# Kernel optimization log

Hardware: AMD Instinct MI355X
Metric: run time of the kernel (lower is better)

The kernel has to match this reference:

```python
import jax, jax.numpy as jnp
import numpy as np

B, S, HID = 2, 2048, 1024
H, HKV, D = 16, 8, 128
G = H // HKV  # GQA group size
EPS = 1e-6
THETA = 1000000.0


def setup_inputs() -> dict:
    key = jax.random.key(0)
    ks = jax.random.split(key, 6)
    hidden_states = jax.random.normal(ks[0], (B, S, HID), dtype=jnp.float32)
    # causal boolean mask: True = attend
    attention_mask = jnp.tril(jnp.ones((S, S), dtype=bool))[None, None]
    # RoPE tables (HF convention: freqs duplicated across both halves)
    inv_freq = 1.0 / (THETA ** (jnp.arange(0, D, 2, dtype=jnp.float32) / D))
    ang = jnp.arange(S, dtype=jnp.float32)[:, None] * inv_freq[None, :]  # [S, D/2]
    emb = jnp.concatenate([ang, ang], axis=-1)  # [S, D]
    cos, sin = jnp.cos(emb), jnp.sin(emb)
    std = 0.02
    Wq = jax.random.normal(ks[1], (HID, H * D), dtype=jnp.float32) * std
    Wk = jax.random.normal(ks[2], (HID, HKV * D), dtype=jnp.float32) * std
    Wv = jax.random.normal(ks[3], (HID, HKV * D), dtype=jnp.float32) * std
    Wo = jax.random.normal(ks[4], (H * D, HID), dtype=jnp.float32) * std
    q_norm_w = jnp.ones((D,), dtype=jnp.float32)
    k_norm_w = jnp.ones((D,), dtype=jnp.float32)
    return {"hidden_states": hidden_states, "attention_mask": attention_mask,
            "cos": cos, "sin": sin, "Wq": Wq, "Wk": Wk, "Wv": Wv, "Wo": Wo,
            "q_norm_w": q_norm_w, "k_norm_w": k_norm_w}


def _rms_norm(x, w):
    var = jnp.mean(x * x, axis=-1, keepdims=True)
    return x * jax.lax.rsqrt(var + EPS) * w


def _rotate_half(x):
    x1, x2 = jnp.split(x, 2, axis=-1)
    return jnp.concatenate([-x2, x1], axis=-1)


def reference(hidden_states, attention_mask, cos, sin, Wq, Wk, Wv, Wo, q_norm_w, k_norm_w):
    b, s, _ = hidden_states.shape
    xq = (hidden_states @ Wq).reshape(b, s, H, D).transpose(0, 2, 1, 3)    # [B,H,S,D]
    xk = (hidden_states @ Wk).reshape(b, s, HKV, D).transpose(0, 2, 1, 3)  # [B,Hkv,S,D]
    xv = (hidden_states @ Wv).reshape(b, s, HKV, D).transpose(0, 2, 1, 3)  # [B,Hkv,S,D]
    xq = _rms_norm(xq, q_norm_w)
    xk = _rms_norm(xk, k_norm_w)
    c = cos[None, None]  # [1,1,S,D]
    si = sin[None, None]
    xq = xq * c + _rotate_half(xq) * si
    xk = xk * c + _rotate_half(xk) * si
    # GQA without materializing repeated KV: group q heads per kv head
    xqg = xq.reshape(b, HKV, G, s, D)
    scale = 1.0 / jnp.sqrt(jnp.asarray(D, dtype=xq.dtype))
    scores = jnp.einsum('bkgsd,bktd->bkgst', xqg, xk) * scale  # [B,Hkv,G,S,S]
    mask = attention_mask[:, :, None]  # [1,1,1,S,S]
    scores = jnp.where(mask, scores, jnp.asarray(-jnp.inf, dtype=scores.dtype))
    probs = jax.nn.softmax(scores, axis=-1)
    out = jnp.einsum('bkgst,bktd->bkgsd', probs, xv)  # [B,Hkv,G,S,D]
    out = out.reshape(b, H, s, D).transpose(0, 2, 1, 3).reshape(b, s, H * D)
    return out @ Wo
```

## Files before the change

### kernel.cpp

```cpp
#include <hip/hip_runtime.h>
#include <stdint.h>

#define B_ 2
#define S_ 2048
#define H_ 16
#define HKV_ 8
#define D_ 128
#define EPS_ 1e-6f
#define SCALE_ 0.08838834764831845f
#define KVSTRIDE_ 262144

typedef __attribute__((ext_vector_type(8))) __bf16 bf16x8;
typedef __attribute__((ext_vector_type(4))) float f32x4;
typedef __attribute__((ext_vector_type(16))) float f32x16;

static __device__ __forceinline__ uint16_t f2b(float f) {
  uint32_t u = __builtin_bit_cast(uint32_t, f);
  u += 0x7fffu + ((u >> 16) & 1u);
  return (uint16_t)(u >> 16);
}
static __device__ __forceinline__ float b2f(uint16_t b) {
  uint32_t u = ((uint32_t)b) << 16;
  return __builtin_bit_cast(float, u);
}

typedef const __attribute__((address_space(1))) uint32_t* gas_p;
typedef __attribute__((address_space(3))) uint32_t* las_p;
static __device__ __forceinline__ void gload16(const void* g, void* l) {
  __builtin_amdgcn_global_load_lds((gas_p)g, (las_p)l, 16, 0, 0);
}

__global__ __launch_bounds__(256) void prep(const float* __restrict__ hidden,
                                            uint16_t* __restrict__ Xb,
                                            const float* __restrict__ Wq,
                                            const float* __restrict__ Wk,
                                            const float* __restrict__ Wv,
                                            const float* __restrict__ Wo,
                                            uint16_t* __restrict__ Wqt,
                                            uint16_t* __restrict__ Wkt,
                                            uint16_t* __restrict__ Wvt,
                                            uint16_t* __restrict__ Wot) {
  __shared__ float tt[32][33];
  int bid = blockIdx.x;
  if (bid < 4096) {
    int i = bid * 256 + threadIdx.x;
    float4 f = ((const float4*)hidden)[i];
    uint2 o;
    o.x = (uint32_t)f2b(f.x) | ((uint32_t)f2b(f.y) << 16);
    o.y = (uint32_t)f2b(f.z) | ((uint32_t)f2b(f.w) << 16);
    ((uint2*)Xb)[i] = o;
    return;
  }
  bid -= 4096;
  const float* src; uint16_t* dst; int K, N, bx, by;
  if (bid < 2048)       { src = Wq; dst = Wqt; K = 1024; N = 2048; bx = bid & 63; by = bid >> 6; }
  else if (bid < 3072)  { bid -= 2048; src = Wk; dst = Wkt; K = 1024; N = 1024; bx = bid & 31; by = bid >> 5; }
  else if (bid < 4096)  { bid -= 3072; src = Wv; dst = Wvt; K = 1024; N = 1024; bx = bid & 31; by = bid >> 5; }
  else                  { bid -= 4096; src = Wo; dst = Wot; K = 2048; N = 1024; bx = bid & 31; by = bid >> 5; }
  int nb = bx * 32, kb = by * 32;
  int tx = threadIdx.x & 31, ty = threadIdx.x >> 5;
  #pragma unroll
  for (int i = ty; i < 32; i += 8) tt[i][tx] = src[(size_t)(kb + i) * N + nb + tx];
  __syncthreads();
  #pragma unroll
  for (int i = ty; i < 32; i += 8) dst[(size_t)(nb + i) * K + kb + tx] = f2b(tt[tx][i]);
}

__global__ __launch_bounds__(256) void gemm_qkv(const uint16_t* __restrict__ A,
                                                const uint16_t* __restrict__ Bt,
                                                uint16_t* __restrict__ Qb,
                                                uint16_t* __restrict__ Kb,
                                                uint16_t* __restrict__ Vtb,
                                                const float* __restrict__ qw,
                                                const float* __restrict__ kw,
                                                const float* __restrict__ cosr,
                                                const float* __restrict__ sinr) {
  __shared__ uint16_t Sh[128 * 128];
  uint16_t* Al = Sh;
  uint16_t* Bl = Sh + 128 * 64;
  int tid = threadIdx.x;
  int lane = tid & 63, lr = lane & 15, g = lane >> 4;
  int w = tid >> 6, wm = w >> 1, wn = w & 1;
  int wbase = w * 64;
  int m0 = blockIdx.y * 128, n0 = blockIdx.x * 128;
  f32x4 acc[4][4] = {};
  for (int k0 = 0; k0 < 1024; k0 += 64) {
    __syncthreads();
    #pragma unroll
    for (int p = 0; p < 4; ++p) {
      int c = tid + p * 256;
      int row = c >> 3, cb = c & 7;
      int sc = (cb ^ (row & 7)) * 8;
      gload16(A + (size_t)(m0 + row) * 1024 + k0 + sc, Al + (size_t)(p * 256 + wbase) * 8);
      gload16(Bt + (size_t)(n0 + row) * 1024 + k0 + sc, Bl + (size_t)(p * 256 + wbase) * 8);
    }
    __syncthreads();
    #pragma unroll
    for (int ks = 0; ks < 2; ++ks) {
      bf16x8 af[4], bfr[4];
      #pragma unroll
      for (int mi = 0; mi < 4; ++mi) {
        int row = wm * 64 + mi * 16 + lr;
        af[mi] = *(bf16x8*)((char*)Al + row * 128 + ((ks * 64 + g * 16) ^ ((row & 7) << 4)));
      }
      #pragma unroll
      for (int ni = 0; ni < 4; ++ni) {
        int row = wn * 64 + ni * 16 + lr;
        bfr[ni] = *(bf16x8*)((char*)Bl + row * 128 + ((ks * 64 + g * 16) ^ ((row & 7) << 4)));
      }
      __builtin_amdgcn_s_setprio(1);
      #pragma unroll
      for (int mi = 0; mi < 4; ++mi)
        #pragma unroll
        for (int ni = 0; ni < 4; ++ni)
          acc[mi][ni] = __builtin_amdgcn_mfma_f32_16x16x32_bf16(af[mi], bfr[ni], acc[mi][ni], 0, 0, 0);
      __builtin_amdgcn_s_setprio(0);
    }
  }
  __syncthreads();
  uint16_t* L = Sh;
  #pragma unroll
  for (int mi = 0; mi < 4; ++mi)
    #pragma unroll
    for (int ni = 0; ni < 4; ++ni)
      #pragma unroll
      for (int e = 0; e < 4; ++e) {
        int row = wm * 64 + mi * 16 + 4 * g + e;
        int col = wn * 64 + ni * 16 + lr;
        L[row * 128 + ((((col >> 3) ^ (row & 7)) << 3) | (col & 7))] = f2b(acc[mi][ni][e]);
      }
  __syncthreads();
  int hsel = n0 >> 7;
  if (hsel < 24) {
    int row = tid >> 1, half = tid & 1;
    int gr = m0 + row, bb = gr >> 11, s = gr & 2047;
    int d0 = half * 32;
    float x[64];
    #pragma unroll
    for (int c8 = 0; c8 < 8; ++c8) {
      int jj = (c8 & 3) * 8 + d0 + (c8 >> 2) * 64;
      union { bf16x8 v; uint16_t u[8]; } tmp;
      tmp.v = *(bf16x8*)(L + row * 128 + (((jj >> 3) ^ (row & 7)) << 3));
      #pragma unroll
      for (int k = 0; k < 8; ++k) x[c8 * 8 + k] = b2f(tmp.u[k]);
    }
    float ss = 0.f;
    #pragma unroll
    for (int k = 0; k < 64; ++k) ss += x[k] * x[k];
    ss += __shfl_xor(ss, 1, 64);
    float rn = rsqrtf(ss * (1.0f / 128.0f) + EPS_);
    const float* wv = (hsel < 16) ? qw : kw;
    float scq = (hsel < 16) ? SCALE_ : 1.0f;
    rn *= scq;
    uint16_t* outp = (hsel < 16)
      ? Qb + (((size_t)(bb * 16 + hsel)) * 2048 + s) * 128
      : Kb + (((size_t)(bb * 8 + (hsel - 16))) * 2048 + s) * 128;
    const float* cR = cosr + s * 128;
    const float* sR = sinr + s * 128;
    #pragma unroll
    for (int c = 0; c < 4; ++c) {
      int dlo = d0 + c * 8;
      uint16_t olo[8], ohi[8];
      #pragma unroll
      for (int k = 0; k < 8; ++k) {
        int d = dlo + k;
        float x1 = x[c * 8 + k] * rn * wv[d];
        float x2 = x[32 + c * 8 + k] * rn * wv[d + 64];
        olo[k] = f2b(x1 * cR[d] - x2 * sR[d]);
        ohi[k] = f2b(x2 * cR[d + 64] + x1 * sR[d + 64]);
      }
      *(uint4*)(outp + dlo) = *(uint4*)olo;
      *(uint4*)(outp + 64 + dlo) = *(uint4*)ohi;
    }
  } else {
    int kvh = hsel - 24;
    int d0 = tid >> 1, sh = tid & 1;
    int bb = m0 >> 11, sg0 = (m0 & 2047) + sh * 64;
    union { uint16_t u[64]; uint4 q[8]; } vv;
    #pragma unroll
    for (int sl = 0; sl < 64; ++sl) {
      int srow = sh * 64 + sl;
      vv.u[sl] = L[srow * 128 + ((((d0 >> 3) ^ (srow & 7)) << 3) | (d0 & 7))];
    }
    uint16_t* vt = Vtb + (((size_t)(bb * 8 + kvh)) * 128 + d0) * 2048 + sg0;
    #pragma unroll
    for (int c = 0; c < 8; ++c) *(uint4*)(vt + c * 8) = vv.q[c];
  }
}

__global__ __launch_bounds__(256) void vrepack(const uint16_t* __restrict__ Vt,
                                               uint16_t* __restrict__ Vp) {
  int bkv = blockIdx.y, p = blockIdx.x;
  const uint16_t* src = Vt + (size_t)bkv * KVSTRIDE_;
  uint16_t* dst = Vp + (size_t)bkv * KVSTRIDE_;
  #pragma unroll
  for (int i = 0; i < 16; ++i) {
    int idx = i * 256 + threadIdx.x;
    int d = idx >> 5, sc = p * 32 + (idx & 31);
    int s8 = sc * 8;
    uint4 v = *(const uint4*)(src + (size_t)d * 2048 + s8);
    int kb64 = s8 >> 6, j = (s8 >> 4) & 3, hh = (s8 >> 3) & 1;
    int dt = d >> 5, qlv = d & 31;
    ((uint4*)dst)[(kb64 * 16 + dt * 4 + j) * 64 + hh * 32 + qlv] = v;
  }
}

__global__ __launch_bounds__(256) void gemm_o(const uint16_t* __restrict__ A,
                                              const uint16_t* __restrict__ Bt,
                                              float* __restrict__ Cout,
                                              int M, int N, int K) {
  __shared__ uint16_t Al[128 * 64];
  __shared__ uint16_t Bl[64 * 64];
  int tid = threadIdx.x;
  int lane = tid & 63, lr = lane & 15, g = lane >> 4;
  int w = tid >> 6, wm = w >> 1, wn = w & 1;
  int wbase = w * 64;
  int m0 = blockIdx.y * 128, n0 = blockIdx.x * 64;
  f32x4 acc[4][2] = {};
  for (int k0 = 0; k0 < K; k0 += 64) {
    __syncthreads();
    #pragma unroll
    for (int p = 0; p < 4; ++p) {
      int c = tid + p * 256;
      int row = c >> 3, cb = c & 7;
      int sc = (cb ^ (row & 7)) * 8;
      gload16(A + (size_t)(m0 + row) * K + k0 + sc, Al + (size_t)(p * 256 + wbase) * 8);
    }
    #pragma unroll
    for (int p = 0; p < 2; ++p) {
      int c = tid + p * 256;
      int row = c >> 3, cb = c & 7;
      int sc = (cb ^ (row & 7)) * 8;
      gload16(Bt + (size_t)(n0 + row) * K + k0 + sc, Bl + (size_t)(p * 256 + wbase) * 8);
    }
    __syncthreads();
    #pragma unroll
    for (int ks = 0; ks < 2; ++ks) {
      bf16x8 af[4], bfr[2];
      #pragma unroll
      for (int mi = 0; mi < 4; ++mi) {
        int row = wm * 64 + mi * 16 + lr;
        af[mi] = *(bf16x8*)((char*)Al + row * 128 + ((ks * 64 + g * 16) ^ ((row & 7) << 4)));
      }
      #pragma unroll
      for (int ni = 0; ni < 2; ++ni) {
        int row = wn * 32 + ni * 16 + lr;
        bfr[ni] = *(bf16x8*)((char*)Bl + row * 128 + ((ks * 64 + g * 16) ^ ((row & 7) << 4)));
      }
      __builtin_amdgcn_s_setprio(1);
      #pragma unroll
      for (int mi = 0; mi < 4; ++mi)
        #pragma unroll
        for (int ni = 0; ni < 2; ++ni)
          acc[mi][ni] = __builtin_amdgcn_mfma_f32_16x16x32_bf16(af[mi], bfr[ni], acc[mi][ni], 0, 0, 0);
      __builtin_amdgcn_s_setprio(0);
    }
  }
  #pragma unroll
  for (int mi = 0; mi < 4; ++mi)
    #pragma unroll
    for (int ni = 0; ni < 2; ++ni)
      #pragma unroll
      for (int e = 0; e < 4; ++e) {
        int row = m0 + wm * 64 + mi * 16 + 4 * g + e;
        int col = n0 + wn * 32 + ni * 16 + lr;
        Cout[(size_t)row * N + col] = acc[mi][ni][e];
      }
}

#define STAGE(BUF, KB) {                                                       \
  int kb64 = (KB) * 64;                                                        \
  _Pragma("unroll") for (int p2 = 0; p2 < 4; ++p2) {                           \
    int ck = p2 * 4 + w;                                                       \
    int krow = ck * 4 + (lane >> 4);                                           \
    int kg = (lane & 15) ^ (krow & 7);                                         \
    gload16(Kg + (size_t)(kb64 + krow) * D_ + kg * 8, Kl[BUF] + ck * 512);     \
  } }

__global__ __launch_bounds__(256, 2) void attn_kernel(const uint16_t* __restrict__ Qb,
                                                      const uint16_t* __restrict__ Kb,
                                                      const uint16_t* __restrict__ Vp,
                                                      uint16_t* __restrict__ out) {
  __shared__ uint16_t Kl[2][64 * 128];
  int tid = threadIdx.x, lane = tid & 63, w = tid >> 6;
  int ql = lane & 31, hi = lane >> 5;
  int bi = blockIdx.x;
  int biH = bi >> 8;
  int j2 = bi & 255;
  int qgl = j2 >> 5;
  int qg = biH ? qgl : 15 - qgl;
  int rem = j2 & 31;
  int bkv = rem >> 1, hsel = rem & 1;
  int b = bkv >> 3, kv = bkv & 7, h = kv * 2 + hsel;
  int qt = qg * 4 + w;
  int q0 = qt * 32;
  int mykb = qt >> 1;
  int kbmax = 2 * qg + 1;
  const uint16_t* Qg = Qb + ((size_t)(b * H_ + h)) * S_ * D_;
  const uint16_t* Kg = Kb + ((size_t)(b * HKV_ + kv)) * S_ * D_;
  const uint16_t* Vpg = Vp + (size_t)(b * HKV_ + kv) * KVSTRIDE_;
  bf16x8 qf[8];
  #pragma unroll
  for (int t = 0; t < 8; ++t)
    qf[t] = *(const bf16x8*)(Qg + (size_t)(q0 + ql) * D_ + t * 16 + 8 * hi);
  f32x16 O[4] = {};
  float mrun = -__builtin_inff();
  float lrun = 0.f;
  STAGE(0, 0)
  for (int kb = 0; kb <= kbmax; ++kb) {
    int cur = kb & 1;
    __syncthreads();
    if (kb < kbmax) STAGE(cur ^ 1, kb + 1)
    if (kb <= mykb) {
      const uint16_t* KlC = Kl[cur];
      const uint16_t* Vb64 = Vpg + (size_t)kb * 8192;
      bool diag = (kb == mykb);
      bool skip2 = diag && ((qt & 1) == 0);
      float p0[16], p1[16];
      {
        bf16x8 kf[8];
        #pragma unroll
        for (int t = 0; t < 8; ++t)
          kf[t] = *(const bf16x8*)(KlC + ql * 128 + (((2 * t + hi) ^ (ql & 7)) * 8));
        f32x16 acc = {};
        __builtin_amdgcn_s_setprio(1);
        #pragma unroll
        for (int t = 0; t < 8; ++t)
          acc = __builtin_amdgcn_mfma_f32_32x32x16_bf16(kf[t], qf[t], acc, 0, 0, 0);
        __builtin_amdgcn_s_setprio(0);
        #pragma unroll
        for (int r = 0; r < 16; ++r) p0[r] = acc[r];
      }
      if (!skip2) {
        bf16x8 kf[8];
        #pragma unroll
        for (int t = 0; t < 8; ++t)
          kf[t] = *(const bf16x8*)(KlC + (32 + ql) * 128 + (((2 * t + hi) ^ (ql & 7)) * 8));
        f32x16 acc = {};
        __builtin_amdgcn_s_setprio(1);
        #pragma unroll
        for (int t = 0; t < 8; ++t)
          acc = __builtin_amdgcn_mfma_f32_32x32x16_bf16(kf[t], qf[t], acc, 0, 0, 0);
        __builtin_amdgcn_s_setprio(0);
        #pragma unroll
        for (int r = 0; r < 16; ++r) p1[r] = acc[r];
      }
      bf16x8 vf[16];
      #pragma unroll
      for (int dt = 0; dt < 4; ++dt) {
        vf[dt * 4 + 0] = *(const bf16x8*)(Vb64 + ((dt * 4 + 0) * 64 + lane) * 8);
        vf[dt * 4 + 1] = *(const bf16x8*)(Vb64 + ((dt * 4 + 1) * 64 + lane) * 8);
      }
      if (!skip2) {
        #pragma unroll
        for (int dt = 0; dt < 4; ++dt) {
          vf[dt * 4 + 2] = *(const bf16x8*)(Vb64 + ((dt * 4 + 2) * 64 + lane) * 8);
          vf[dt * 4 + 3] = *(const bf16x8*)(Vb64 + ((dt * 4 + 3) * 64 + lane) * 8);
        }
      }
      if (diag && !(qt & 1)) {
        #pragma unroll
        for (int r = 0; r < 16; ++r) {
          int kk = kb * 64 + 8 * (r >> 2) + 4 * hi + (r & 3);
          if (kk > q0 + ql) p0[r] = -__builtin_inff();
        }
      }
      if (diag && (qt & 1)) {
        #pragma unroll
        for (int r = 0; r < 16; ++r) {
          int kk = kb * 64 + 32 + 8 * (r >> 2) + 4 * hi + (r & 3);
          if (kk > q0 + ql) p1[r] = -__builtin_inff();
        }
      }
      float m8[8];
      #pragma unroll
      for (int i = 0; i < 8; ++i) m8[i] = fmaxf(p0[i], p0[i + 8]);
      if (!skip2) {
        #pragma unroll
        for (int i = 0; i < 8; ++i) m8[i] = fmaxf(m8[i], fmaxf(p1[i], p1[i + 8]));
      }
      float m4a = fmaxf(m8[0], m8[4]), m4b = fmaxf(m8[1], m8[5]);
      float m4c = fmaxf(m8[2], m8[6]), m4d = fmaxf(m8[3], m8[7]);
      float pmax = fmaxf(fmaxf(m4a, m4b), fmaxf(m4c, m4d));
      pmax = fmaxf(pmax, __shfl_xor(pmax, 32, 64));
      if (__any(pmax > mrun + 8.f)) {
        float mnew = fmaxf(mrun, pmax);
        float rs = __expf(mrun - mnew);
        lrun *= rs;
        #pragma unroll
        for (int r = 0; r < 16; ++r) {
          float rr = __shfl(rs, (r & 3) + 8 * (r >> 2) + 4 * hi, 64);
          #pragma unroll
          for (int dt = 0; dt < 4; ++dt) O[dt][r] *= rr;
        }
        mrun = mnew;
      }
      float ls = 0.f;
      union PW { uint32_t w[4]; bf16x8 v; } pa0, pa1;
      #pragma unroll
      for (int r = 0; r < 16; ++r) { p0[r] = __expf(p0[r] - mrun); ls += p0[r]; }
      {
        uint32_t uu[4][2];
        #pragma unroll
        for (int T = 0; T < 4; ++T) {
          asm("v_cvt_pk_bf16_f32 %0, %1, %2" : "=v"(uu[T][0]) : "v"(p0[4 * T]), "v"(p0[4 * T + 1]));
          asm("v_cvt_pk_bf16_f32 %0, %1, %2" : "=v"(uu[T][1]) : "v"(p0[4 * T + 2]), "v"(p0[4 * T + 3]));
        }
        uint32_t a = uu[0][0], bb2 = uu[1][0];
        asm("v_permlane32_swap_b32 %0, %1" : "+v"(a), "+v"(bb2));
        uint32_t c = uu[0][1], d = uu[1][1];
        asm("v_permlane32_swap_b32 %0, %1" : "+v"(c), "+v"(d));
        pa0.w[0] = a; pa0.w[1] = c; pa0.w[2] = bb2; pa0.w[3] = d;
        uint32_t a2 = uu[2][0], b2 = uu[3][0];
        asm("v_permlane32_swap_b32 %0, %1" : "+v"(a2), "+v"(b2));
        uint32_t c2 = uu[2][1], d2 = uu[3][1];
        asm("v_permlane32_swap_b32 %0, %1" : "+v"(c2), "+v"(d2));
        pa1.w[0] = a2; pa1.w[1] = c2; pa1.w[2] = b2; pa1.w[3] = d2;
      }
      __builtin_amdgcn_s_setprio(1);
      #pragma unroll
      for (int dt = 0; dt < 4; ++dt) {
        O[dt] = __builtin_amdgcn_mfma_f32_32x32x16_bf16(pa0.v, vf[dt * 4 + 0], O[dt], 0, 0, 0);
        O[dt] = __builtin_amdgcn_mfma_f32_32x32x16_bf16(pa1.v, vf[dt * 4 + 1], O[dt], 0, 0, 0);
      }
      __builtin_amdgcn_s_setprio(0);
      if (!skip2) {
        union PW pa2, pa3;
        #pragma unroll
        for (int r = 0; r < 16; ++r) { p1[r] = __expf(p1[r] - mrun); ls += p1[r]; }
        {
          uint32_t uu[4][2];
          #pragma unroll
          for (int T = 0; T < 4; ++T) {
            asm("v_cvt_pk_bf16_f32 %0, %1, %2" : "=v"(uu[T][0]) : "v"(p1[4 * T]), "v"(p1[4 * T + 1]));
            asm("v_cvt_pk_bf16_f32 %0, %1, %2" : "=v"(uu[T][1]) : "v"(p1[4 * T + 2]), "v"(p1[4 * T + 3]));
          }
          uint32_t a = uu[0][0], bb2 = uu[1][0];
          asm("v_permlane32_swap_b32 %0, %1" : "+v"(a), "+v"(bb2));
          uint32_t c = uu[0][1], d = uu[1][1];
          asm("v_permlane32_swap_b32 %0, %1" : "+v"(c), "+v"(d));
          pa2.w[0] = a; pa2.w[1] = c; pa2.w[2] = bb2; pa2.w[3] = d;
          uint32_t a2 = uu[2][0], b2 = uu[3][0];
          asm("v_permlane32_swap_b32 %0, %1" : "+v"(a2), "+v"(b2));
          uint32_t c2 = uu[2][1], d2 = uu[3][1];
          asm("v_permlane32_swap_b32 %0, %1" : "+v"(c2), "+v"(d2));
          pa3.w[0] = a2; pa3.w[1] = c2; pa3.w[2] = b2; pa3.w[3] = d2;
        }
        __builtin_amdgcn_s_setprio(1);
        #pragma unroll
        for (int dt = 0; dt < 4; ++dt) {
          O[dt] = __builtin_amdgcn_mfma_f32_32x32x16_bf16(pa2.v, vf[dt * 4 + 2], O[dt], 0, 0, 0);
          O[dt] = __builtin_amdgcn_mfma_f32_32x32x16_bf16(pa3.v, vf[dt * 4 + 3], O[dt], 0, 0, 0);
        }
        __builtin_amdgcn_s_setprio(0);
      }
      ls += __shfl_xor(ls, 32, 64);
      lrun += ls;
    }
  }
  float linv = 1.0f / lrun;
  #pragma unroll
  for (int r = 0; r < 16; ++r) {
    int qrl = (r & 3) + 8 * (r >> 2) + 4 * hi;
    float lr_ = __shfl(linv, qrl, 64);
    #pragma unroll
    for (int dt = 0; dt < 4; ++dt) {
      size_t o = ((size_t)(b * S_ + q0 + qrl)) * 2048 + h * 128 + dt * 32 + ql;
      out[o] = f2b(O[dt][r] * lr_);
    }
  }
}

extern "C" void kernel_launch(void* const* d_in, const int* in_sizes, int n_in,
                              void* d_out, int out_size, void* d_ws, size_t ws_size,
                              hipStream_t stream) {
  const float* hidden = (const float*)d_in[0];
  const float* cosr = (const float*)d_in[2];
  const float* sinr = (const float*)d_in[3];
  const float* Wq = (const float*)d_in[4];
  const float* Wk = (const float*)d_in[5];
  const float* Wv = (const float*)d_in[6];
  const float* Wo = (const float*)d_in[7];
  const float* qw = (const float*)d_in[8];
  const float* kw = (const float*)d_in[9];

  uint16_t* p = (uint16_t*)d_ws;
  uint16_t* Xb   = p; p += (size_t)4096 * 1024;
  uint16_t* Wqt  = p; p += (size_t)2048 * 1024;
  uint16_t* Wkt  = p; p += (size_t)1024 * 1024;
  uint16_t* Wvt  = p; p += (size_t)1024 * 1024;
  uint16_t* Wot  = p; p += (size_t)1024 * 2048;
  uint16_t* Qbuf = p; p += (size_t)B_ * H_ * S_ * D_;
  uint16_t* Kbuf = p; p += (size_t)B_ * HKV_ * S_ * D_;
  uint16_t* Vtb  = p; p += (size_t)B_ * HKV_ * S_ * D_;
  uint16_t* attn = p; p += (size_t)4096 * 2048;
  uint16_t* Vpb  = Xb;

  prep<<<10240, 256, 0, stream>>>(hidden, Xb, Wq, Wk, Wv, Wo, Wqt, Wkt, Wvt, Wot);
  gemm_qkv<<<dim3(32, 32), 256, 0, stream>>>(Xb, Wqt, Qbuf, Kbuf, Vtb, qw, kw, cosr, sinr);
  vrepack<<<dim3(8, 16), 256, 0, stream>>>(Vtb, Vpb);
  attn_kernel<<<512, 256, 0, stream>>>(Qbuf, Kbuf, Vpb, attn);
  gemm_o<<<dim3(16, 32), 256, 0, stream>>>(attn, Wot, (float*)d_out, 4096, 1024, 2048);
}
```

Before: 174.7 us.

## Split causal KV range across wave pairs and merge partial softmax states

Each attention block now covers two 32-row query tiles. Its four waves split into two halves that walk the low and high parts of the causal KV range in 32-key steps, and the halves merge their partial O, max and sum through shared memory at the end. The grid doubles to 1024 blocks and launch bounds allow 4 blocks per CU, which should balance the causal triangle and raise occupancy. In exchange it adds a shared-memory merge pass with an extra barrier, and the smaller 32-key steps mean more loop overhead and more softmax rescale bookkeeping per key.

```diff
diff --git a/kernel.cpp b/kernel.cpp
--- a/kernel.cpp
+++ b/kernel.cpp
@@ -268,34 +268,34 @@
       }
 }
 
-#define STAGE(BUF, KB) {                                                       \
-  int kb64 = (KB) * 64;                                                        \
-  _Pragma("unroll") for (int p2 = 0; p2 < 4; ++p2) {                           \
-    int ck = p2 * 4 + w;                                                       \
-    int krow = ck * 4 + (lane >> 4);                                           \
-    int kg = (lane & 15) ^ (krow & 7);                                         \
-    gload16(Kg + (size_t)(kb64 + krow) * D_ + kg * 8, Kl[BUF] + ck * 512);     \
+#define STAGE2(BUF, ITN) {                                                       \
+  int klo = (ITN); int khi = nlow + (ITN);                                       \
+  _Pragma("unroll") for (int p2 = 0; p2 < 4; ++p2) {                             \
+    int stream = p2 >> 1;                                                        \
+    int ci = (p2 & 1) * 4 + w;                                                   \
+    int row = ci * 4 + (lane >> 4);                                              \
+    int kg = (lane & 15) ^ (row & 7);                                            \
+    int kb = stream ? khi : klo;                                                 \
+    gload16(Kg + (size_t)(kb * 32 + row) * D_ + kg * 8,                          \
+            (uint16_t*)smem + ((BUF) * 2 + stream) * 4096 + ci * 512);           \
   } }
 
-__global__ __launch_bounds__(256, 2) void attn_kernel(const uint16_t* __restrict__ Qb,
+__global__ __launch_bounds__(256, 4) void attn_kernel(const uint16_t* __restrict__ Qb,
                                                       const uint16_t* __restrict__ Kb,
                                                       const uint16_t* __restrict__ Vp,
                                                       uint16_t* __restrict__ out) {
-  __shared__ uint16_t Kl[2][64 * 128];
+  __shared__ __attribute__((aligned(16))) uint8_t smem[33280];
   int tid = threadIdx.x, lane = tid & 63, w = tid >> 6;
   int ql = lane & 31, hi = lane >> 5;
   int bi = blockIdx.x;
-  int biH = bi >> 8;
-  int j2 = bi & 255;
-  int qgl = j2 >> 5;
-  int qg = biH ? qgl : 15 - qgl;
-  int rem = j2 & 31;
+  int pr = 31 - (bi >> 5);
+  int rem = bi & 31;
   int bkv = rem >> 1, hsel = rem & 1;
   int b = bkv >> 3, kv = bkv & 7, h = kv * 2 + hsel;
-  int qt = qg * 4 + w;
+  int qt = pr * 2 + (w & 1);
+  int half = w >> 1;
   int q0 = qt * 32;
-  int mykb = qt >> 1;
-  int kbmax = 2 * qg + 1;
+  int nlow = pr + 1;
   const uint16_t* Qg = Qb + ((size_t)(b * H_ + h)) * S_ * D_;
   const uint16_t* Kg = Kb + ((size_t)(b * HKV_ + kv)) * S_ * D_;
   const uint16_t* Vpg = Vp + (size_t)(b * HKV_ + kv) * KVSTRIDE_;
@@ -306,17 +306,18 @@
   f32x16 O[4] = {};
   float mrun = -__builtin_inff();
   float lrun = 0.f;
-  STAGE(0, 0)
-  for (int kb = 0; kb <= kbmax; ++kb) {
-    int cur = kb & 1;
+  STAGE2(0, 0)
+  for (int it = 0; it <= pr; ++it) {
+    int cur = it & 1;
     __syncthreads();
-    if (kb < kbmax) STAGE(cur ^ 1, kb + 1)
-    if (kb <= mykb) {
-      const uint16_t* KlC = Kl[cur];
-      const uint16_t* Vb64 = Vpg + (size_t)kb * 8192;
-      bool diag = (kb == mykb);
-      bool skip2 = diag && ((qt & 1) == 0);
-      float p0[16], p1[16];
+    if (it < pr) STAGE2(cur ^ 1, it + 1)
+    int kb = half ? nlow + it : it;
+    if (!half || kb <= qt) {
+      const uint16_t* KlC = (const uint16_t*)smem + (cur * 2 + half) * 4096;
+      const uint16_t* Vb64 = Vpg + (size_t)(kb >> 1) * 8192;
+      int j0 = (kb & 1) * 2;
+      bool diag = (kb == qt);
+      float p0[16];
       {
         bf16x8 kf[8];
         #pragma unroll
@@ -331,54 +332,22 @@
         #pragma unroll
         for (int r = 0; r < 16; ++r) p0[r] = acc[r];
       }
-      if (!skip2) {
-        bf16x8 kf[8];
-        #pragma unroll
-        for (int t = 0; t < 8; ++t)
-          kf[t] = *(const bf16x8*)(KlC + (32 + ql) * 128 + (((2 * t + hi) ^ (ql & 7)) * 8));
-        f32x16 acc = {};
-        __builtin_amdgcn_s_setprio(1);
-        #pragma unroll
-        for (int t = 0; t < 8; ++t)
-          acc = __builtin_amdgcn_mfma_f32_32x32x16_bf16(kf[t], qf[t], acc, 0, 0, 0);
-        __builtin_amdgcn_s_setprio(0);
-        #pragma unroll
-        for (int r = 0; r < 16; ++r) p1[r] = acc[r];
-      }
-      bf16x8 vf[16];
+      bf16x8 vf0[4], vf1[4];
       #pragma unroll
       for (int dt = 0; dt < 4; ++dt) {
-        vf[dt * 4 + 0] = *(const bf16x8*)(Vb64 + ((dt * 4 + 0) * 64 + lane) * 8);
-        vf[dt * 4 + 1] = *(const bf16x8*)(Vb64 + ((dt * 4 + 1) * 64 + lane) * 8);
-      }
-      if (!skip2) {
-        #pragma unroll
-        for (int dt = 0; dt < 4; ++dt) {
-          vf[dt * 4 + 2] = *(const bf16x8*)(Vb64 + ((dt * 4 + 2) * 64 + lane) * 8);
-          vf[dt * 4 + 3] = *(const bf16x8*)(Vb64 + ((dt * 4 + 3) * 64 + lane) * 8);
-        }
-      }
-      if (diag && !(qt & 1)) {
+        vf0[dt] = *(const bf16x8*)(Vb64 + ((dt * 4 + j0 + 0) * 64 + lane) * 8);
+        vf1[dt] = *(const bf16x8*)(Vb64 + ((dt * 4 + j0 + 1) * 64 + lane) * 8);
+      }
+      if (diag) {
         #pragma unroll
         for (int r = 0; r < 16; ++r) {
-          int kk = kb * 64 + 8 * (r >> 2) + 4 * hi + (r & 3);
+          int kk = kb * 32 + 8 * (r >> 2) + 4 * hi + (r & 3);
           if (kk > q0 + ql) p0[r] = -__builtin_inff();
         }
       }
-      if (diag && (qt & 1)) {
-        #pragma unroll
-        for (int r = 0; r < 16; ++r) {
-          int kk = kb * 64 + 32 + 8 * (r >> 2) + 4 * hi + (r & 3);
-          if (kk > q0 + ql) p1[r] = -__builtin_inff();
-        }
-      }
       float m8[8];
       #pragma unroll
       for (int i = 0; i < 8; ++i) m8[i] = fmaxf(p0[i], p0[i + 8]);
-      if (!skip2) {
-        #pragma unroll
-        for (int i = 0; i < 8; ++i) m8[i] = fmaxf(m8[i], fmaxf(p1[i], p1[i + 8]));
-      }
       float m4a = fmaxf(m8[0], m8[4]), m4b = fmaxf(m8[1], m8[5]);
       float m4c = fmaxf(m8[2], m8[6]), m4d = fmaxf(m8[3], m8[7]);
       float pmax = fmaxf(fmaxf(m4a, m4b), fmaxf(m4c, m4d));
@@ -396,9 +365,9 @@
         mrun = mnew;
       }
       float ls = 0.f;
+      #pragma unroll
+      for (int r = 0; r < 16; ++r) { p0[r] = __expf(p0[r] - mrun); ls += p0[r]; }
       union PW { uint32_t w[4]; bf16x8 v; } pa0, pa1;
-      #pragma unroll
-      for (int r = 0; r < 16; ++r) { p0[r] = __expf(p0[r] - mrun); ls += p0[r]; }
       {
         uint32_t uu[4][2];
         #pragma unroll
@@ -420,53 +389,46 @@
       __builtin_amdgcn_s_setprio(1);
       #pragma unroll
       for (int dt = 0; dt < 4; ++dt) {
-        O[dt] = __builtin_amdgcn_mfma_f32_32x32x16_bf16(pa0.v, vf[dt * 4 + 0], O[dt], 0, 0, 0);
-        O[dt] = __builtin_amdgcn_mfma_f32_32x32x16_bf16(pa1.v, vf[dt * 4 + 1], O[dt], 0, 0, 0);
+        O[dt] = __builtin_amdgcn_mfma_f32_32x32x16_bf16(pa0.v, vf0[dt], O[dt], 0, 0, 0);
+        O[dt] = __builtin_amdgcn_mfma_f32_32x32x16_bf16(pa1.v, vf1[dt], O[dt], 0, 0, 0);
       }
       __builtin_amdgcn_s_setprio(0);
-      if (!skip2) {
-        union PW pa2, pa3;
-        #pragma unroll
-        for (int r = 0; r < 16; ++r) { p1[r] = __expf(p1[r] - mrun); ls += p1[r]; }
-        {
-          uint32_t uu[4][2];
-          #pragma unroll
-          for (int T = 0; T < 4; ++T) {
-            asm("v_cvt_pk_bf16_f32 %0, %1, %2" : "=v"(uu[T][0]) : "v"(p1[4 * T]), "v"(p1[4 * T + 1]));
-            asm("v_cvt_pk_bf16_f32 %0, %1, %2" : "=v"(uu[T][1]) : "v"(p1[4 * T + 2]), "v"(p1[4 * T + 3]));
-          }
-          uint32_t a = uu[0][0], bb2 = uu[1][0];
-          asm("v_permlane32_swap_b32 %0, %1" : "+v"(a), "+v"(bb2));
-          uint32_t c = uu[0][1], d = uu[1][1];
-          asm("v_permlane32_swap_b32 %0, %1" : "+v"(c), "+v"(d));
-          pa2.w[0] = a; pa2.w[1] = c; pa2.w[2] = bb2; pa2.w[3] = d;
-          uint32_t a2 = uu[2][0], b2 = uu[3][0];
-          asm("v_permlane32_swap_b32 %0, %1" : "+v"(a2), "+v"(b2));
-          uint32_t c2 = uu[2][1], d2 = uu[3][1];
-          asm("v_permlane32_swap_b32 %0, %1" : "+v"(c2), "+v"(d2));
-          pa3.w[0] = a2; pa3.w[1] = c2; pa3.w[2] = b2; pa3.w[3] = d2;
-        }
-        __builtin_amdgcn_s_setprio(1);
-        #pragma unroll
-        for (int dt = 0; dt < 4; ++dt) {
-          O[dt] = __builtin_amdgcn_mfma_f32_32x32x16_bf16(pa2.v, vf[dt * 4 + 2], O[dt], 0, 0, 0);
-          O[dt] = __builtin_amdgcn_mfma_f32_32x32x16_bf16(pa3.v, vf[dt * 4 + 3], O[dt], 0, 0, 0);
-        }
-        __builtin_amdgcn_s_setprio(0);
-      }
       ls += __shfl_xor(ls, 32, 64);
       lrun += ls;
     }
   }
-  float linv = 1.0f / lrun;
-  #pragma unroll
-  for (int r = 0; r < 16; ++r) {
-    int qrl = (r & 3) + 8 * (r >> 2) + 4 * hi;
-    float lr_ = __shfl(linv, qrl, 64);
-    #pragma unroll
-    for (int dt = 0; dt < 4; ++dt) {
-      size_t o = ((size_t)(b * S_ + q0 + qrl)) * 2048 + h * 128 + dt * 32 + ql;
-      out[o] = f2b(O[dt][r] * lr_);
+  __syncthreads();
+  float* Om = (float*)smem;
+  float* Ml = (float*)(smem + 32768);
+  int slot = w & 1;
+  if (half) {
+    #pragma unroll
+    for (int r = 0; r < 16; ++r) {
+      int qrl = (r & 3) + 8 * (r >> 2) + 4 * hi;
+      #pragma unroll
+      for (int dt = 0; dt < 4; ++dt)
+        Om[slot * 4096 + qrl * 128 + dt * 32 + ql] = O[dt][r];
+    }
+    if (hi == 0) { Ml[slot * 64 + ql * 2] = mrun; Ml[slot * 64 + ql * 2 + 1] = lrun; }
+  }
+  __syncthreads();
+  if (!half) {
+    float m2 = Ml[slot * 64 + ql * 2], l2 = Ml[slot * 64 + ql * 2 + 1];
+    float mn = fmaxf(mrun, m2);
+    float a1 = __expf(mrun - mn), a2 = __expf(m2 - mn);
+    float lfin = lrun * a1 + l2 * a2;
+    float linv = 1.0f / lfin;
+    #pragma unroll
+    for (int r = 0; r < 16; ++r) {
+      int qrl = (r & 3) + 8 * (r >> 2) + 4 * hi;
+      float a1r = __shfl(a1, qrl, 64);
+      float a2r = __shfl(a2, qrl, 64);
+      float lr_ = __shfl(linv, qrl, 64);
+      #pragma unroll
+      for (int dt = 0; dt < 4; ++dt) {
+        float v = O[dt][r] * a1r + Om[slot * 4096 + qrl * 128 + dt * 32 + ql] * a2r;
+        out[((size_t)(b * S_ + q0 + qrl)) * 2048 + h * 128 + dt * 32 + ql] = f2b(v * lr_);
+      }
     }
   }
 }
@@ -499,6 +461,6 @@
   prep<<<10240, 256, 0, stream>>>(hidden, Xb, Wq, Wk, Wv, Wo, Wqt, Wkt, Wvt, Wot);
   gemm_qkv<<<dim3(32, 32), 256, 0, stream>>>(Xb, Wqt, Qbuf, Kbuf, Vtb, qw, kw, cosr, sinr);
   vrepack<<<dim3(8, 16), 256, 0, stream>>>(Vtb, Vpb);
-  attn_kernel<<<512, 256, 0, stream>>>(Qbuf, Kbuf, Vpb, attn);
+  attn_kernel<<<1024, 256, 0, stream>>>(Qbuf, Kbuf, Vpb, attn);
   gemm_o<<<dim3(16, 32), 256, 0, stream>>>(attn, Wot, (float*)d_out, 4096, 1024, 2048);
 }
```

New measurement: 384.1 us. +119.8%, slower.
